# Kernel tuning notes

Hardware: AMD Instinct MI355X
Metric: run time of the kernel (lower is better)

The kernel has to match this reference:

```python
import jax, jax.numpy as jnp
import numpy as np

SPAN_W = 8      # fixed span width (tokens per span)
HID = 150       # Score hidden dim (hardcoded in source)


def _score_mlp(x, w1, b1, w2, b2, w3, b3):
    # Linear->ReLU->(Dropout=id)->Linear->ReLU->(Dropout=id)->Linear ; out dim 1
    h = jax.nn.relu(x @ w1 + b1)
    h = jax.nn.relu(h @ w2 + b2)
    return h @ w3 + b3


def _make_mlp_params(key, in_dim):
    ks = jax.random.split(key, 6)
    s1 = 1.0 / np.sqrt(in_dim)
    s2 = 1.0 / np.sqrt(HID)
    return (
        jax.random.uniform(ks[0], (in_dim, HID), jnp.float32, -s1, s1),
        jax.random.uniform(ks[1], (HID,), jnp.float32, -s1, s1),
        jax.random.uniform(ks[2], (HID, HID), jnp.float32, -s2, s2),
        jax.random.uniform(ks[3], (HID,), jnp.float32, -s2, s2),
        jax.random.uniform(ks[4], (HID, 1), jnp.float32, -s2, s2),
        jax.random.uniform(ks[5], (1,), jnp.float32, -s2, s2),
    )


def setup_inputs() -> dict:
    key = jax.random.key(0)
    k_emb, k_sp, k_a, k_m, k_p = jax.random.split(key, 5)
    E = 768
    B, T, S = 2, 2048, 96
    encoded_docs = jax.random.normal(k_emb, (B, T, E), jnp.float32)
    span_starts = jnp.sort(
        jax.random.randint(k_sp, (B, S), 0, 2040, dtype=jnp.int64), axis=-1)
    aw1, ab1, aw2, ab2, aw3, ab3 = _make_mlp_params(k_a, E)          # attn Score
    mw1, mb1, mw2, mb2, mw3, mb3 = _make_mlp_params(k_m, 3 * E)      # mention Score
    pw1, pb1, pw2, pb2, pw3, pb3 = _make_mlp_params(k_p, 9 * E)      # pair Score
    return {
        "encoded_docs": encoded_docs, "span_starts": span_starts,
        "aw1": aw1, "ab1": ab1, "aw2": aw2, "ab2": ab2, "aw3": aw3, "ab3": ab3,
        "mw1": mw1, "mb1": mb1, "mw2": mw2, "mb2": mb2, "mw3": mw3, "mb3": mb3,
        "pw1": pw1, "pb1": pb1, "pw2": pw2, "pb2": pb2, "pw3": pw3, "pb3": pb3,
    }


def reference(encoded_docs, span_starts,
              aw1, ab1, aw2, ab2, aw3, ab3,
              mw1, mb1, mw2, mb2, mw3, mb3,
              pw1, pb1, pw2, pb2, pw3, pb3):
    B, T, E = encoded_docs.shape
    S = span_starts.shape[1]

    # --- MentionScore ---
    attns = _score_mlp(encoded_docs, aw1, ab1, aw2, ab2, aw3, ab3)  # [B,T,1]
    starts = span_starts                                              # [B,S]
    ends = starts + (SPAN_W - 1)
    g_start = jnp.take_along_axis(encoded_docs, starts[:, :, None], axis=1)  # [B,S,E]
    g_end = jnp.take_along_axis(encoded_docs, ends[:, :, None], axis=1)      # [B,S,E]
    tok_idx = starts[:, :, None] + jnp.arange(SPAN_W, dtype=starts.dtype)     # [B,S,W]
    flat = tok_idx.reshape(B, S * SPAN_W)
    span_emb = jnp.take_along_axis(encoded_docs, flat[:, :, None], axis=1).reshape(B, S, SPAN_W, E)
    span_attn = jnp.take_along_axis(attns, flat[:, :, None], axis=1).reshape(B, S, SPAN_W, 1)
    g_attn = jnp.sum(span_emb * span_attn, axis=2)                    # [B,S,E]
    g_i = jnp.concatenate([g_start, g_end, g_attn], axis=-1)          # [B,S,3E]
    mention_scores = _score_mlp(g_i, mw1, mb1, mw2, mb2, mw3, mb3)    # [B,S,1]

    # --- PairwiseScore: all pairs (i=span_1, j=span_2) ---
    gi = jnp.broadcast_to(g_i[:, :, None, :], (B, S, S, 3 * E))
    gj = jnp.broadcast_to(g_i[:, None, :, :], (B, S, S, 3 * E))
    pair = jnp.concatenate([gi, gj, gi * gj], axis=-1)                # [B,S,S,9E]
    pair_scores = _score_mlp(pair, pw1, pb1, pw2, pb2, pw3, pb3)      # [B,S,S,1]
    ext = (mention_scores[:, :, None, :] + mention_scores[:, None, :, :] + pair_scores) / 3.0
    return jnp.clip(ext, 0.0, 1.0)
```

## Files before the change

### kernel.cpp

```cpp
#include <hip/hip_runtime.h>

#define EDIM   768
#define E3     2304
#define HIDD   150
#define TT     2048
#define SS     96
#define BB     2

typedef unsigned short u16;
using frag   = __attribute__((ext_vector_type(8))) short;
using f32x4v = __attribute__((ext_vector_type(4))) float;
using u16x8  = __attribute__((ext_vector_type(8))) unsigned short;

__device__ __forceinline__ u16 bf16rn(float f) {
    union { float f; unsigned u; } v; v.f = f;
    unsigned r = v.u + 0x7FFF + ((v.u >> 16) & 1);
    return (u16)(r >> 16);
}
__device__ __forceinline__ float bf16tof(u16 h) {
    union { unsigned u; float f; } v; v.u = ((unsigned)h) << 16;
    return v.f;
}
__device__ __forceinline__ void split2(float f, u16& hi, u16& lo) {
    hi = bf16rn(f); lo = bf16rn(f - bf16tof(hi));
}
__device__ __forceinline__ int swzoff(int row, int qd) {
    return row * 32 + (((qd + (row >> 1)) & 3) << 3);
}
__device__ __forceinline__ void async16(const void* g, void* l) {
    __builtin_amdgcn_global_load_lds(
        (const __attribute__((address_space(1))) void*)g,
        (__attribute__((address_space(3))) void*)l, 16, 0, 0);
}

__global__ __launch_bounds__(256) void k_prep_all(
    const float* __restrict__ pw1, const float* __restrict__ mw1,
    const float* __restrict__ aw1, const float* __restrict__ aw2,
    const float* __restrict__ pw2, const float* __restrict__ mw2,
    u16* __restrict__ W12t_hi, u16* __restrict__ W12t_lo,
    u16* __restrict__ AW1t_hi, u16* __restrict__ AW1t_lo,
    u16* __restrict__ AW2t_hi, u16* __restrict__ AW2t_lo,
    u16* __restrict__ PW2t_hi, u16* __restrict__ PW2t_lo,
    u16* __restrict__ MW2t_hi, u16* __restrict__ MW2t_lo)
{
    __shared__ float tile[64][33];
    const int bi = blockIdx.x;
    const int t  = threadIdx.x;

    if (bi < 720) {
        const int k0 = (bi % 36) * 64;
        const int n0 = (bi / 36) * 32;
        const int seg = n0 / 160;
        const int nloc0 = n0 - seg * 160;
        for (int idx = t; idx < 2048; idx += 256) {
            const int kk = idx >> 5, nn = idx & 31;
            const int nl = nloc0 + nn;
            const int k  = k0 + kk;
            float v = 0.f;
            if (nl < HIDD) {
                if (seg == 0)      v = pw1[(long)k * HIDD + nl];
                else if (seg == 1) v = pw1[(long)(E3 + k) * HIDD + nl];
                else if (seg == 2) v = mw1[(long)k * HIDD + nl];
                else               v = pw1[(long)(2 * E3 + k) * HIDD + nl];
            }
            tile[kk][nn] = v;
        }
        __syncthreads();
        for (int idx = t; idx < 2048; idx += 256) {
            const int nn = idx >> 6, kk = idx & 63;
            u16 hi, lo; split2(tile[kk][nn], hi, lo);
            W12t_hi[(long)(n0 + nn) * E3 + k0 + kk] = hi;
            W12t_lo[(long)(n0 + nn) * E3 + k0 + kk] = lo;
        }
    } else if (bi < 1488) {
        const int k = bi - 720;
        if (t < 160) {
            float v = (t < HIDD) ? aw1[k * HIDD + t] : 0.f;
            u16 hi, lo; split2(v, hi, lo);
            AW1t_hi[(long)t * EDIM + k] = hi;
            AW1t_lo[(long)t * EDIM + k] = lo;
        }
    } else {
        const int r = bi - 1488;
        const int k = r % 160;
        const int which = r / 160;
        const float* src = (which == 0) ? aw2 : (which == 1) ? pw2 : mw2;
        u16* dh = (which == 0) ? AW2t_hi : (which == 1) ? PW2t_hi : MW2t_hi;
        u16* dl = (which == 0) ? AW2t_lo : (which == 1) ? PW2t_lo : MW2t_lo;
        if (t < 160) {
            float v = (t < HIDD && k < HIDD) ? src[k * HIDD + t] : 0.f;
            u16 hi, lo; split2(v, hi, lo);
            dh[t * 160 + k] = hi;
            dl[t * 160 + k] = lo;
        }
    }
}

__global__ __launch_bounds__(256) void k_attn1(
    const float* __restrict__ X, const int* __restrict__ spans,
    const u16* __restrict__ AW1t_hi, const u16* __restrict__ AW1t_lo,
    float* __restrict__ AH1)
{
    __shared__ __align__(16) u16 As_hi[32 * 40];
    __shared__ __align__(16) u16 As_lo[32 * 40];
    __shared__ __align__(16) u16 Bs_hi[160 * 40];
    __shared__ __align__(16) u16 Bs_lo[160 * 40];

    const int t    = threadIdx.x;
    const int lane = t & 63;
    const int m    = lane & 15;
    const int quad = lane >> 4;
    const int w    = t >> 6;
    const int mt   = (w & 1) * 16;
    const int nb   = (w >> 1) * 80;
    const int ks   = blockIdx.y;

    const int rr = t >> 3, q = t & 7;
    const int grow = blockIdx.x * 32 + rr;
    const int bs = grow >> 3, sw = grow & 7;
    const int b  = bs / SS;
    const int tok = spans[bs] + sw;
    const float* arow = X + ((long)b * TT + tok) * EDIM;

    f32x4v acc[5];
    #pragma unroll
    for (int ht = 0; ht < 5; ++ht)
        #pragma unroll
        for (int r = 0; r < 4; ++r) acc[ht][r] = 0.f;

    for (int tt = 0; tt < 6; ++tt) {
        const int kk0 = ks * 192 + tt * 32;
        {
            const float4 xv = *(const float4*)&arow[kk0 + q * 4];
            ushort4 hv, lv;
            split2(xv.x, hv.x, lv.x); split2(xv.y, hv.y, lv.y);
            split2(xv.z, hv.z, lv.z); split2(xv.w, hv.w, lv.w);
            *(ushort4*)&As_hi[rr * 40 + q * 4] = hv;
            *(ushort4*)&As_lo[rr * 40 + q * 4] = lv;
        }
        #pragma unroll
        for (int it = 0; it < 3; ++it) {
            const int v = t + it * 256;
            if (v < 640) {
                const int h = v >> 2, qq = v & 3;
                *(uint4*)&Bs_hi[h * 40 + qq * 8] = *(const uint4*)&AW1t_hi[(long)h * EDIM + kk0 + qq * 8];
                *(uint4*)&Bs_lo[h * 40 + qq * 8] = *(const uint4*)&AW1t_lo[(long)h * EDIM + kk0 + qq * 8];
            }
        }
        __syncthreads();
        const frag ah = *(const frag*)&As_hi[(mt + m) * 40 + quad * 8];
        const frag al = *(const frag*)&As_lo[(mt + m) * 40 + quad * 8];
        #pragma unroll
        for (int ht = 0; ht < 5; ++ht) {
            const frag bh = *(const frag*)&Bs_hi[(nb + ht * 16 + m) * 40 + quad * 8];
            const frag bl = *(const frag*)&Bs_lo[(nb + ht * 16 + m) * 40 + quad * 8];
            acc[ht] = __builtin_amdgcn_mfma_f32_16x16x32_bf16(al, bh, acc[ht], 0, 0, 0);
            acc[ht] = __builtin_amdgcn_mfma_f32_16x16x32_bf16(ah, bl, acc[ht], 0, 0, 0);
            acc[ht] = __builtin_amdgcn_mfma_f32_16x16x32_bf16(ah, bh, acc[ht], 0, 0, 0);
        }
        __syncthreads();
    }
    #pragma unroll
    for (int ht = 0; ht < 5; ++ht) {
        #pragma unroll
        for (int r = 0; r < 4; ++r) {
            const int row = blockIdx.x * 32 + mt + quad * 4 + r;
            const int col = nb + ht * 16 + m;
            if (col < HIDD) atomicAdd(&AH1[row * 160 + col], acc[ht][r]);
        }
    }
}

__global__ __launch_bounds__(256) void k_attn2(
    const float* __restrict__ AH1,
    const u16* __restrict__ AW2t_hi, const u16* __restrict__ AW2t_lo,
    const float* __restrict__ ab1, const float* __restrict__ ab2,
    const float* __restrict__ aw3, const float* __restrict__ ab3,
    float* __restrict__ attn_g)
{
    __shared__ __align__(16) u16 As_hi[32 * 40];
    __shared__ __align__(16) u16 As_lo[32 * 40];
    __shared__ __align__(16) u16 Bs_hi[160 * 40];
    __shared__ __align__(16) u16 Bs_lo[160 * 40];
    __shared__ float h1s[32 * 160];
    __shared__ float red[32];

    const int t    = threadIdx.x;
    const int lane = t & 63;
    const int m    = lane & 15;
    const int quad = lane >> 4;
    const int w    = t >> 6;
    const int mt   = (w & 1) * 16;
    const int nb   = (w >> 1) * 80;

    for (int u = t; u < 1280; u += 256) {
        const int row = u / 40, c4 = u - (u / 40) * 40;
        const int c0 = c4 * 4;
        const float4 v = *(const float4*)&AH1[(blockIdx.x * 32 + row) * 160 + c0];
        h1s[row * 160 + c0 + 0] = (c0 + 0 < HIDD) ? fmaxf(v.x + ab1[c0 + 0], 0.f) : 0.f;
        h1s[row * 160 + c0 + 1] = (c0 + 1 < HIDD) ? fmaxf(v.y + ab1[c0 + 1], 0.f) : 0.f;
        h1s[row * 160 + c0 + 2] = (c0 + 2 < HIDD) ? fmaxf(v.z + ab1[c0 + 2], 0.f) : 0.f;
        h1s[row * 160 + c0 + 3] = (c0 + 3 < HIDD) ? fmaxf(v.w + ab1[c0 + 3], 0.f) : 0.f;
    }
    if (t < 32) red[t] = 0.f;
    __syncthreads();

    const int rr = t >> 3, q = t & 7;
    f32x4v acc2[5];
    #pragma unroll
    for (int ht = 0; ht < 5; ++ht)
        #pragma unroll
        for (int r = 0; r < 4; ++r) acc2[ht][r] = 0.f;

    for (int kk = 0; kk < 5; ++kk) {
        {
            const float4 xv = *(const float4*)&h1s[rr * 160 + kk * 32 + q * 4];
            ushort4 hv, lv;
            split2(xv.x, hv.x, lv.x); split2(xv.y, hv.y, lv.y);
            split2(xv.z, hv.z, lv.z); split2(xv.w, hv.w, lv.w);
            *(ushort4*)&As_hi[rr * 40 + q * 4] = hv;
            *(ushort4*)&As_lo[rr * 40 + q * 4] = lv;
        }
        #pragma unroll
        for (int it = 0; it < 3; ++it) {
            const int v = t + it * 256;
            if (v < 640) {
                const int h = v >> 2, qq = v & 3;
                *(uint4*)&Bs_hi[h * 40 + qq * 8] = *(const uint4*)&AW2t_hi[h * 160 + kk * 32 + qq * 8];
                *(uint4*)&Bs_lo[h * 40 + qq * 8] = *(const uint4*)&AW2t_lo[h * 160 + kk * 32 + qq * 8];
            }
        }
        __syncthreads();
        const frag ah = *(const frag*)&As_hi[(mt + m) * 40 + quad * 8];
        const frag al = *(const frag*)&As_lo[(mt + m) * 40 + quad * 8];
        #pragma unroll
        for (int ht = 0; ht < 5; ++ht) {
            const frag bh = *(const frag*)&Bs_hi[(nb + ht * 16 + m) * 40 + quad * 8];
            const frag bl = *(const frag*)&Bs_lo[(nb + ht * 16 + m) * 40 + quad * 8];
            acc2[ht] = __builtin_amdgcn_mfma_f32_16x16x32_bf16(al, bh, acc2[ht], 0, 0, 0);
            acc2[ht] = __builtin_amdgcn_mfma_f32_16x16x32_bf16(ah, bl, acc2[ht], 0, 0, 0);
            acc2[ht] = __builtin_amdgcn_mfma_f32_16x16x32_bf16(ah, bh, acc2[ht], 0, 0, 0);
        }
        __syncthreads();
    }

    float s[4] = {0.f, 0.f, 0.f, 0.f};
    #pragma unroll
    for (int ht = 0; ht < 5; ++ht) {
        const int col = nb + ht * 16 + m;
        if (col < HIDD) {
            const float w3 = aw3[col];
            #pragma unroll
            for (int r = 0; r < 4; ++r)
                s[r] += fmaxf(acc2[ht][r] + ab2[col], 0.f) * w3;
        }
    }
    #pragma unroll
    for (int r = 0; r < 4; ++r) {
        for (int off = 8; off > 0; off >>= 1) s[r] += __shfl_down(s[r], off, 16);
    }
    if (m == 0) {
        #pragma unroll
        for (int r = 0; r < 4; ++r) atomicAdd(&red[mt + quad * 4 + r], s[r]);
    }
    __syncthreads();
    if (t < 32) attn_g[blockIdx.x * 32 + t] = red[t] + ab3[0];
}

__global__ __launch_bounds__(256) void k_span_g(
    const float* __restrict__ X, const int* __restrict__ spans,
    const float* __restrict__ attn_g, float* __restrict__ G_ws,
    u16* __restrict__ Gs_hi, u16* __restrict__ Gs_lo)
{
    __shared__ float a8[8];
    const int t  = threadIdx.x;
    const int bs = blockIdx.x;
    const int b  = bs / SS;
    const int start = spans[bs];
    const float* xb = X + ((long)b * TT + start) * EDIM;
    float* Gp = G_ws + (long)bs * E3;
    u16* Gh = Gs_hi + (long)bs * E3;
    u16* Gl = Gs_lo + (long)bs * E3;
    if (t < 8) a8[t] = attn_g[bs * 8 + t];
    __syncthreads();

    for (int e = t; e < EDIM; e += 256) {
        const float gs = xb[e];
        const float ge = xb[7 * EDIM + e];
        float ga = 0.f;
        #pragma unroll
        for (int w = 0; w < 8; ++w) ga += xb[w * EDIM + e] * a8[w];
        Gp[e] = gs; Gp[EDIM + e] = ge; Gp[2 * EDIM + e] = ga;
        u16 hi, lo;
        split2(gs, hi, lo); Gh[e] = hi;            Gl[e] = lo;
        split2(ge, hi, lo); Gh[EDIM + e] = hi;     Gl[EDIM + e] = lo;
        split2(ga, hi, lo); Gh[2 * EDIM + e] = hi; Gl[2 * EDIM + e] = lo;
    }
}

__global__ __launch_bounds__(256) void k_heavy(
    const float* __restrict__ G_ws,
    const u16* __restrict__ Gs_hi, const u16* __restrict__ Gs_lo,
    const u16* __restrict__ W12t_hi, const u16* __restrict__ W12t_lo,
    const u16* __restrict__ PCt_hi, const u16* __restrict__ PCt_lo,
    float* __restrict__ H1parts, float* __restrict__ UVM)
{
    __shared__ __align__(16) char smem[48128];
    const int id = blockIdx.x;
    const int t  = threadIdx.x;
    const int lane = t & 63;
    const int m    = lane & 15;
    const int quad = lane >> 4;
    const int w    = t >> 6;

    if (id < 576) {
        float* gis  = (float*)smem;
        float* gjst = (float*)(smem + 3072);
        u16* As_hi  = (u16*)(smem + 15360);
        u16* As_lo  = (u16*)(smem + 21504);
        u16* Bs_hi  = (u16*)(smem + 27648);
        u16* Bs_lo  = (u16*)(smem + 37888);

        const int ks = id % 3;
        const int i  = (id / 3) % SS;
        const int b  = id / 288;
        const int ksbase = ks * 768;
        const int jt0 = i >> 4;
        const int ntiles = 6 - jt0;
        const int j0 = jt0 * 16;
        const int R  = 96 - j0;
        const int nI = R >> 3;

        const int hb   = (w & 1) * 80;
        const int apar = w >> 1;
        const int Bl_h = lane >> 2;
        const int Bl_c = lane & 3;
        const int gj_r = lane >> 3;
        const int gj_c = lane & 7;

        const float* Gi = G_ws + (long)(b * SS + i) * E3 + ksbase;
        for (int e = t; e < 768; e += 256) gis[e] = Gi[e];

        f32x4v acc[3][5];
        #pragma unroll
        for (int jt = 0; jt < 3; ++jt)
            #pragma unroll
            for (int ht = 0; ht < 5; ++ht)
                #pragma unroll
                for (int r = 0; r < 4; ++r) acc[jt][ht][r] = 0.f;

        for (int tt = 0; tt < 24; ++tt) {
            const int kk0 = ksbase + tt * 32;
            for (int q2 = w; q2 < 10; q2 += 4) {
                const int h  = q2 * 16 + Bl_h;
                const int qd = (Bl_c - (h >> 1)) & 3;
                const long so = (long)h * E3 + kk0 + qd * 8;
                async16(&PCt_hi[so], &Bs_hi[q2 * 512]);
                async16(&PCt_lo[so], &Bs_lo[q2 * 512]);
            }
            for (int g2 = w; g2 < nI; g2 += 4) {
                const int row = j0 + g2 * 8 + gj_r;
                async16(&G_ws[(long)(b * SS + row) * E3 + kk0 + gj_c * 4],
                        &gjst[g2 * 256]);
            }
            __syncthreads();

            for (int u = t; u < R * 4; u += 256) {
                const int rr = u >> 2, qd = u & 3;
                const float4 g0 = *(const float4*)&gjst[rr * 32 + qd * 8];
                const float4 g1 = *(const float4*)&gjst[rr * 32 + qd * 8 + 4];
                const int kl = tt * 32 + qd * 8;
                u16x8 hv, lv; u16 h, l;
                split2(g0.x * gis[kl + 0], h, l); hv[0] = h; lv[0] = l;
                split2(g0.y * gis[kl + 1], h, l); hv[1] = h; lv[1] = l;
                split2(g0.z * gis[kl + 2], h, l); hv[2] = h; lv[2] = l;
                split2(g0.w * gis[kl + 3], h, l); hv[3] = h; lv[3] = l;
                split2(g1.x * gis[kl + 4], h, l); hv[4] = h; lv[4] = l;
                split2(g1.y * gis[kl + 5], h, l); hv[5] = h; lv[5] = l;
                split2(g1.z * gis[kl + 6], h, l); hv[6] = h; lv[6] = l;
                split2(g1.w * gis[kl + 7], h, l); hv[7] = h; lv[7] = l;
                const int o = swzoff(rr, qd);
                *(u16x8*)&As_hi[o] = hv;
                *(u16x8*)&As_lo[o] = lv;
            }
            __syncthreads();

            frag ah[3], al[3];
            #pragma unroll
            for (int u = 0; u < 3; ++u) {
                const int a = apar + 2 * u;
                if (a < ntiles) {
                    const int o = swzoff(a * 16 + m, quad);
                    ah[u] = *(const frag*)&As_hi[o];
                    al[u] = *(const frag*)&As_lo[o];
                }
            }
            #pragma unroll
            for (int ht = 0; ht < 5; ++ht) {
                const int o = swzoff(hb + ht * 16 + m, quad);
                const frag bh = *(const frag*)&Bs_hi[o];
                const frag bl = *(const frag*)&Bs_lo[o];
                #pragma unroll
                for (int u = 0; u < 3; ++u) {
                    if (apar + 2 * u < ntiles) {
                        acc[u][ht] = __builtin_amdgcn_mfma_f32_16x16x32_bf16(al[u], bh, acc[u][ht], 0, 0, 0);
                        acc[u][ht] = __builtin_amdgcn_mfma_f32_16x16x32_bf16(ah[u], bl, acc[u][ht], 0, 0, 0);
                        acc[u][ht] = __builtin_amdgcn_mfma_f32_16x16x32_bf16(ah[u], bh, acc[u][ht], 0, 0, 0);
                    }
                }
            }
            __syncthreads();
        }

        float* dst = H1parts + (long)ks * ((long)BB * SS * SS * 160);
        #pragma unroll
        for (int u = 0; u < 3; ++u) {
            const int a = apar + 2 * u;
            if (a < ntiles) {
                #pragma unroll
                for (int ht = 0; ht < 5; ++ht) {
                    #pragma unroll
                    for (int r = 0; r < 4; ++r) {
                        const int j = (jt0 + a) * 16 + quad * 4 + r;
                        const int h = hb + ht * 16 + m;
                        dst[((long)(b * SS + i) * SS + j) * 160 + h] = acc[u][ht][r];
                    }
                }
            }
        }
    } else {
        u16* As_hi = (u16*)smem;
        u16* As_lo = (u16*)(smem + 5120);
        u16* Bs_hi = (u16*)(smem + 10240);
        u16* Bs_lo = (u16*)(smem + 23040);

        const int u0 = id - 576;
        const int mb = u0 % 3;
        const int nb = (u0 / 3) % 3;
        const int kz = u0 / 9;
        const int mhalf = (w & 1) * 32;
        const int nbase = (w >> 1) * 80;
        const int arr = t >> 2, aq = t & 3;

        f32x4v acc[2][5];
        #pragma unroll
        for (int i = 0; i < 2; ++i)
            #pragma unroll
            for (int j = 0; j < 5; ++j)
                #pragma unroll
                for (int r = 0; r < 4; ++r) acc[i][j][r] = 0.f;

        for (int tt = 0; tt < 6; ++tt) {
            const int kk0 = kz * 192 + tt * 32;
            *(uint4*)&As_hi[arr * 40 + aq * 8] = *(const uint4*)&Gs_hi[(long)(mb * 64 + arr) * E3 + kk0 + aq * 8];
            *(uint4*)&As_lo[arr * 40 + aq * 8] = *(const uint4*)&Gs_lo[(long)(mb * 64 + arr) * E3 + kk0 + aq * 8];
            #pragma unroll
            for (int it = 0; it < 3; ++it) {
                const int v = t + it * 256;
                if (v < 640) {
                    const int h = v >> 2, qq = v & 3;
                    *(uint4*)&Bs_hi[h * 40 + qq * 8] = *(const uint4*)&W12t_hi[(long)(nb * 160 + h) * E3 + kk0 + qq * 8];
                    *(uint4*)&Bs_lo[h * 40 + qq * 8] = *(const uint4*)&W12t_lo[(long)(nb * 160 + h) * E3 + kk0 + qq * 8];
                }
            }
            __syncthreads();
            frag ah[2], al[2];
            #pragma unroll
            for (int mt = 0; mt < 2; ++mt) {
                ah[mt] = *(const frag*)&As_hi[(mhalf + mt * 16 + m) * 40 + quad * 8];
                al[mt] = *(const frag*)&As_lo[(mhalf + mt * 16 + m) * 40 + quad * 8];
            }
            #pragma unroll
            for (int ht = 0; ht < 5; ++ht) {
                const frag bh = *(const frag*)&Bs_hi[(nbase + ht * 16 + m) * 40 + quad * 8];
                const frag bl = *(const frag*)&Bs_lo[(nbase + ht * 16 + m) * 40 + quad * 8];
                #pragma unroll
                for (int mt = 0; mt < 2; ++mt) {
                    acc[mt][ht] = __builtin_amdgcn_mfma_f32_16x16x32_bf16(al[mt], bh, acc[mt][ht], 0, 0, 0);
                    acc[mt][ht] = __builtin_amdgcn_mfma_f32_16x16x32_bf16(ah[mt], bl, acc[mt][ht], 0, 0, 0);
                    acc[mt][ht] = __builtin_amdgcn_mfma_f32_16x16x32_bf16(ah[mt], bh, acc[mt][ht], 0, 0, 0);
                }
            }
            __syncthreads();
        }
        float* dst = UVM + (long)nb * (192 * 160);
        #pragma unroll
        for (int mt = 0; mt < 2; ++mt) {
            #pragma unroll
            for (int ht = 0; ht < 5; ++ht) {
                #pragma unroll
                for (int r = 0; r < 4; ++r) {
                    const int row = mb * 64 + mhalf + mt * 16 + quad * 4 + r;
                    const int c   = nbase + ht * 16 + m;
                    atomicAdd(&dst[row * 160 + c], acc[mt][ht][r]);
                }
            }
        }
    }
}

__global__ __launch_bounds__(256) void k_pair2(
    const float* __restrict__ H1parts,
    const float* __restrict__ U_ws, const float* __restrict__ V_ws,
    const float* __restrict__ pb1, const float* __restrict__ m_ws,
    const u16* __restrict__ PW2t_hi, const u16* __restrict__ PW2t_lo,
    const float* __restrict__ pb2, const float* __restrict__ pw3,
    const float* __restrict__ pb3,
    float* __restrict__ out)
{
    __shared__ __align__(16) u16 As_hi[32 * 168];
    __shared__ __align__(16) u16 As_lo[32 * 168];
    __shared__ __align__(16) u16 Bs_hi[160 * 40];
    __shared__ __align__(16) u16 Bs_lo[160 * 40];
    __shared__ float uv[160];
    __shared__ float red[32];

    const long partsz = (long)BB * SS * SS * 160;
    const int t  = threadIdx.x;
    const int js = blockIdx.x;
    const int bi = blockIdx.y;
    const int b  = bi / SS;
    const int ii = bi - b * SS;
    const int jb0 = js * 32;

    if (t < 160) uv[t] = U_ws[bi * 160 + t] + ((t < HIDD) ? pb1[t] : 0.f);
    if (t < 32) red[t] = 0.f;
    __syncthreads();

    for (int u = t; u < 32 * 40; u += 256) {
        const int jl = u / 40, hq = u - (u / 40) * 40;
        const int j  = jb0 + jl;
        const int h0 = hq * 4;
        const int mn = ii < j ? ii : j;
        const int mx = ii < j ? j : ii;
        const long idx = (((long)b * SS + mn) * SS + mx) * 160 + h0;
        const float4 vv = *(const float4*)&V_ws[(b * SS + j) * 160 + h0];
        const float4 a0 = *(const float4*)&H1parts[idx];
        const float4 a1 = *(const float4*)&H1parts[partsz + idx];
        const float4 a2 = *(const float4*)&H1parts[2 * partsz + idx];
        const float p0 = fmaxf(a0.x + a1.x + a2.x + vv.x + uv[h0 + 0], 0.f);
        const float p1 = fmaxf(a0.y + a1.y + a2.y + vv.y + uv[h0 + 1], 0.f);
        const float p2 = fmaxf(a0.z + a1.z + a2.z + vv.z + uv[h0 + 2], 0.f);
        const float p3 = fmaxf(a0.w + a1.w + a2.w + vv.w + uv[h0 + 3], 0.f);
        ushort4 hv, lv;
        split2(p0, hv.x, lv.x); split2(p1, hv.y, lv.y);
        split2(p2, hv.z, lv.z); split2(p3, hv.w, lv.w);
        *(ushort4*)&As_hi[jl * 168 + h0] = hv;
        *(ushort4*)&As_lo[jl * 168 + h0] = lv;
    }
    __syncthreads();

    const int lane = t & 63;
    const int m    = lane & 15;
    const int quad = lane >> 4;
    const int w    = t >> 6;
    const int jt   = w >> 1;
    const int nbs  = (w & 1) * 80;

    f32x4v acc[5];
    #pragma unroll
    for (int ht = 0; ht < 5; ++ht)
        #pragma unroll
        for (int r = 0; r < 4; ++r) acc[ht][r] = 0.f;

    for (int kk = 0; kk < 5; ++kk) {
        #pragma unroll
        for (int it = 0; it < 3; ++it) {
            const int v = t + it * 256;
            if (v < 640) {
                const int n = v >> 2, qq = v & 3;
                *(uint4*)&Bs_hi[n * 40 + qq * 8] = *(const uint4*)&PW2t_hi[n * 160 + kk * 32 + qq * 8];
                *(uint4*)&Bs_lo[n * 40 + qq * 8] = *(const uint4*)&PW2t_lo[n * 160 + kk * 32 + qq * 8];
            }
        }
        __syncthreads();
        const frag ah = *(const frag*)&As_hi[(jt * 16 + m) * 168 + kk * 32 + quad * 8];
        const frag al = *(const frag*)&As_lo[(jt * 16 + m) * 168 + kk * 32 + quad * 8];
        #pragma unroll
        for (int ht = 0; ht < 5; ++ht) {
            const frag bh = *(const frag*)&Bs_hi[(nbs + ht * 16 + m) * 40 + quad * 8];
            const frag bl = *(const frag*)&Bs_lo[(nbs + ht * 16 + m) * 40 + quad * 8];
            acc[ht] = __builtin_amdgcn_mfma_f32_16x16x32_bf16(al, bh, acc[ht], 0, 0, 0);
            acc[ht] = __builtin_amdgcn_mfma_f32_16x16x32_bf16(ah, bl, acc[ht], 0, 0, 0);
            acc[ht] = __builtin_amdgcn_mfma_f32_16x16x32_bf16(ah, bh, acc[ht], 0, 0, 0);
        }
        __syncthreads();
    }

    float s[4] = {0.f, 0.f, 0.f, 0.f};
    #pragma unroll
    for (int ht = 0; ht < 5; ++ht) {
        const int col = nbs + ht * 16 + m;
        if (col < HIDD) {
            const float w3 = pw3[col];
            const float b2 = pb2[col];
            #pragma unroll
            for (int r = 0; r < 4; ++r)
                s[r] += fmaxf(acc[ht][r] + b2, 0.f) * w3;
        }
    }
    #pragma unroll
    for (int r = 0; r < 4; ++r)
        for (int off = 8; off > 0; off >>= 1)
            s[r] += __shfl_down(s[r], off, 16);
    if (m == 0) {
        #pragma unroll
        for (int r = 0; r < 4; ++r)
            atomicAdd(&red[jt * 16 + quad * 4 + r], s[r]);
    }
    __syncthreads();

    if (t < 32) {
        const int j = jb0 + t;
        const float sc = red[t] + pb3[0];
        const float v = (m_ws[bi] + m_ws[b * SS + j] + sc) * (1.f / 3.f);
        out[(long)bi * SS + j] = fminf(fmaxf(v, 0.f), 1.f);
    }
}

extern "C" void kernel_launch(void* const* d_in, const int* in_sizes, int n_in,
                              void* d_out, int out_size, void* d_ws, size_t ws_size,
                              hipStream_t stream)
{
    const float* X     = (const float*)d_in[0];
    const int*   spans = (const int*)  d_in[1];
    const float* aw1 = (const float*)d_in[2];
    const float* ab1 = (const float*)d_in[3];
    const float* aw2 = (const float*)d_in[4];
    const float* ab2 = (const float*)d_in[5];
    const float* aw3 = (const float*)d_in[6];
    const float* ab3 = (const float*)d_in[7];
    const float* mw1 = (const float*)d_in[8];
    const float* mb1 = (const float*)d_in[9];
    const float* mw2 = (const float*)d_in[10];
    const float* mb2 = (const float*)d_in[11];
    const float* mw3 = (const float*)d_in[12];
    const float* mb3 = (const float*)d_in[13];
    const float* pw1 = (const float*)d_in[14];
    const float* pb1 = (const float*)d_in[15];
    const float* pw2 = (const float*)d_in[16];
    const float* pb2 = (const float*)d_in[17];
    const float* pw3 = (const float*)d_in[18];
    const float* pb3 = (const float*)d_in[19];
    float* out = (float*)d_out;

    char* p = (char*)d_ws;
    float* attn_g  = (float*)p;  p += 6144;
    float* G_ws    = (float*)p;  p += (long)442368 * 4;
    u16*   Gs_hi   = (u16*)p;    p += (long)442368 * 2;
    u16*   Gs_lo   = (u16*)p;    p += (long)442368 * 2;
    float* UVM     = (float*)p;  p += (long)3 * 192 * 160 * 4;
    float* AH1     = (float*)p;  p += (long)1536 * 160 * 4;
    float* m_ws    = (float*)p;  p += 1024;
    u16*   W12t_hi = (u16*)p;    p += (long)640 * E3 * 2;
    u16*   W12t_lo = (u16*)p;    p += (long)640 * E3 * 2;
    u16*   AW1t_hi = (u16*)p;    p += (long)160 * EDIM * 2;
    u16*   AW1t_lo = (u16*)p;    p += (long)160 * EDIM * 2;
    u16*   AW2t_hi = (u16*)p;    p += 160 * 160 * 2;
    u16*   AW2t_lo = (u16*)p;    p += 160 * 160 * 2;
    u16*   PW2t_hi = (u16*)p;    p += 160 * 160 * 2;
    u16*   PW2t_lo = (u16*)p;    p += 160 * 160 * 2;
    u16*   MW2t_hi = (u16*)p;    p += 160 * 160 * 2;
    u16*   MW2t_lo = (u16*)p;    p += 160 * 160 * 2;
    float* H1parts = (float*)p;

    float* U_ws = UVM;
    float* V_ws = UVM + 192 * 160;
    float* M_ws = UVM + 2 * 192 * 160;
    const u16* PCt_hi = W12t_hi + (long)480 * E3;
    const u16* PCt_lo = W12t_lo + (long)480 * E3;

    hipMemsetAsync(UVM, 0, ((size_t)3 * 192 * 160 + (size_t)1536 * 160) * sizeof(float), stream);

    k_prep_all<<<dim3(1968), 256, 0, stream>>>(pw1, mw1, aw1, aw2, pw2, mw2,
                                               W12t_hi, W12t_lo, AW1t_hi, AW1t_lo,
                                               AW2t_hi, AW2t_lo, PW2t_hi, PW2t_lo,
                                               MW2t_hi, MW2t_lo);

    k_attn1<<<dim3(48, 4), 256, 0, stream>>>(X, spans, AW1t_hi, AW1t_lo, AH1);
    k_attn2<<<dim3(48), 256, 0, stream>>>(AH1, AW2t_hi, AW2t_lo, ab1, ab2, aw3, ab3, attn_g);
    k_span_g<<<dim3(BB * SS), 256, 0, stream>>>(X, spans, attn_g, G_ws, Gs_hi, Gs_lo);

    k_heavy<<<dim3(684), 256, 0, stream>>>(G_ws, Gs_hi, Gs_lo, W12t_hi, W12t_lo,
                                           PCt_hi, PCt_lo, H1parts, UVM);

    k_attn2<<<dim3(6), 256, 0, stream>>>(M_ws, MW2t_hi, MW2t_lo, mb1, mb2, mw3, mb3, m_ws);

    k_pair2<<<dim3(3, BB * SS), 256, 0, stream>>>(
        H1parts, U_ws, V_ws, pb1, m_ws, PW2t_hi, PW2t_lo, pb2, pw3, pb3, out);
}
```

Before: 215.6 us.

## Fuse attention layer-1 GEMM with weight prep into one heterogeneous launch

Splits the aw1 transpose/split into its own small kernel, then merges the attention first-layer GEMM blocks with the remaining weight-prep blocks in one grid. The attention GEMM now uses a 6-way K split (288 blocks) instead of 4-way, so it runs concurrently with independent weight conversion work. This lets the GEMM overlap with prep and gives it more parallelism, at the cost of more atomic adds into AH1 and one extra small launch.

```diff
diff --git a/kernel.cpp b/kernel.cpp
--- a/kernel.cpp
+++ b/kernel.cpp
@@ -33,21 +33,106 @@
         (__attribute__((address_space(3))) void*)l, 16, 0, 0);
 }
 
-__global__ __launch_bounds__(256) void k_prep_all(
+__global__ __launch_bounds__(256) void k_prep_aw1(
+    const float* __restrict__ aw1, u16* __restrict__ W_hi, u16* __restrict__ W_lo)
+{
+    const int k = blockIdx.x, t = threadIdx.x;
+    if (t < 160) {
+        float v = (t < HIDD) ? aw1[k * HIDD + t] : 0.f;
+        u16 hi, lo; split2(v, hi, lo);
+        W_hi[(long)t * EDIM + k] = hi;
+        W_lo[(long)t * EDIM + k] = lo;
+    }
+}
+
+__global__ __launch_bounds__(256) void k_fused1(
+    const float* __restrict__ X, const int* __restrict__ spans,
+    const u16* __restrict__ AW1t_hi, const u16* __restrict__ AW1t_lo,
+    float* __restrict__ AH1,
     const float* __restrict__ pw1, const float* __restrict__ mw1,
-    const float* __restrict__ aw1, const float* __restrict__ aw2,
-    const float* __restrict__ pw2, const float* __restrict__ mw2,
+    const float* __restrict__ aw2, const float* __restrict__ pw2,
+    const float* __restrict__ mw2,
     u16* __restrict__ W12t_hi, u16* __restrict__ W12t_lo,
-    u16* __restrict__ AW1t_hi, u16* __restrict__ AW1t_lo,
     u16* __restrict__ AW2t_hi, u16* __restrict__ AW2t_lo,
     u16* __restrict__ PW2t_hi, u16* __restrict__ PW2t_lo,
     u16* __restrict__ MW2t_hi, u16* __restrict__ MW2t_lo)
 {
-    __shared__ float tile[64][33];
-    const int bi = blockIdx.x;
+    __shared__ __align__(16) char smem[32768];
+    const int id = blockIdx.x;
     const int t  = threadIdx.x;
 
-    if (bi < 720) {
+    if (id < 288) {
+        u16* As_hi = (u16*)smem;
+        u16* As_lo = (u16*)(smem + 2560);
+        u16* Bs_hi = (u16*)(smem + 5120);
+        u16* Bs_lo = (u16*)(smem + 17920);
+
+        const int lane = t & 63;
+        const int m    = lane & 15;
+        const int quad = lane >> 4;
+        const int w    = t >> 6;
+        const int mt   = (w & 1) * 16;
+        const int nb   = (w >> 1) * 80;
+        const int rb   = id % 48;
+        const int ks   = id / 48;
+
+        const int rr = t >> 3, q = t & 7;
+        const int grow = rb * 32 + rr;
+        const int bs = grow >> 3, sw = grow & 7;
+        const int b  = bs / SS;
+        const int tok = spans[bs] + sw;
+        const float* arow = X + ((long)b * TT + tok) * EDIM;
+
+        f32x4v acc[5];
+        #pragma unroll
+        for (int ht = 0; ht < 5; ++ht)
+            #pragma unroll
+            for (int r = 0; r < 4; ++r) acc[ht][r] = 0.f;
+
+        for (int tt = 0; tt < 4; ++tt) {
+            const int kk0 = ks * 128 + tt * 32;
+            {
+                const float4 xv = *(const float4*)&arow[kk0 + q * 4];
+                ushort4 hv, lv;
+                split2(xv.x, hv.x, lv.x); split2(xv.y, hv.y, lv.y);
+                split2(xv.z, hv.z, lv.z); split2(xv.w, hv.w, lv.w);
+                *(ushort4*)&As_hi[rr * 40 + q * 4] = hv;
+                *(ushort4*)&As_lo[rr * 40 + q * 4] = lv;
+            }
+            #pragma unroll
+            for (int it = 0; it < 3; ++it) {
+                const int v = t + it * 256;
+                if (v < 640) {
+                    const int h = v >> 2, qq = v & 3;
+                    *(uint4*)&Bs_hi[h * 40 + qq * 8] = *(const uint4*)&AW1t_hi[(long)h * EDIM + kk0 + qq * 8];
+                    *(uint4*)&Bs_lo[h * 40 + qq * 8] = *(const uint4*)&AW1t_lo[(long)h * EDIM + kk0 + qq * 8];
+                }
+            }
+            __syncthreads();
+            const frag ah = *(const frag*)&As_hi[(mt + m) * 40 + quad * 8];
+            const frag al = *(const frag*)&As_lo[(mt + m) * 40 + quad * 8];
+            #pragma unroll
+            for (int ht = 0; ht < 5; ++ht) {
+                const frag bh = *(const frag*)&Bs_hi[(nb + ht * 16 + m) * 40 + quad * 8];
+                const frag bl = *(const frag*)&Bs_lo[(nb + ht * 16 + m) * 40 + quad * 8];
+                acc[ht] = __builtin_amdgcn_mfma_f32_16x16x32_bf16(al, bh, acc[ht], 0, 0, 0);
+                acc[ht] = __builtin_amdgcn_mfma_f32_16x16x32_bf16(ah, bl, acc[ht], 0, 0, 0);
+                acc[ht] = __builtin_amdgcn_mfma_f32_16x16x32_bf16(ah, bh, acc[ht], 0, 0, 0);
+            }
+            __syncthreads();
+        }
+        #pragma unroll
+        for (int ht = 0; ht < 5; ++ht) {
+            #pragma unroll
+            for (int r = 0; r < 4; ++r) {
+                const int row = rb * 32 + mt + quad * 4 + r;
+                const int col = nb + ht * 16 + m;
+                if (col < HIDD) atomicAdd(&AH1[row * 160 + col], acc[ht][r]);
+            }
+        }
+    } else if (id < 1008) {
+        float (*tile)[33] = (float(*)[33])smem;
+        const int bi = id - 288;
         const int k0 = (bi % 36) * 64;
         const int n0 = (bi / 36) * 32;
         const int seg = n0 / 160;
@@ -72,16 +157,8 @@
             W12t_hi[(long)(n0 + nn) * E3 + k0 + kk] = hi;
             W12t_lo[(long)(n0 + nn) * E3 + k0 + kk] = lo;
         }
-    } else if (bi < 1488) {
-        const int k = bi - 720;
-        if (t < 160) {
-            float v = (t < HIDD) ? aw1[k * HIDD + t] : 0.f;
-            u16 hi, lo; split2(v, hi, lo);
-            AW1t_hi[(long)t * EDIM + k] = hi;
-            AW1t_lo[(long)t * EDIM + k] = lo;
-        }
     } else {
-        const int r = bi - 1488;
+        const int r = id - 1008;
         const int k = r % 160;
         const int which = r / 160;
         const float* src = (which == 0) ? aw2 : (which == 1) ? pw2 : mw2;
@@ -92,81 +169,6 @@
             u16 hi, lo; split2(v, hi, lo);
             dh[t * 160 + k] = hi;
             dl[t * 160 + k] = lo;
-        }
-    }
-}
-
-__global__ __launch_bounds__(256) void k_attn1(
-    const float* __restrict__ X, const int* __restrict__ spans,
-    const u16* __restrict__ AW1t_hi, const u16* __restrict__ AW1t_lo,
-    float* __restrict__ AH1)
-{
-    __shared__ __align__(16) u16 As_hi[32 * 40];
-    __shared__ __align__(16) u16 As_lo[32 * 40];
-    __shared__ __align__(16) u16 Bs_hi[160 * 40];
-    __shared__ __align__(16) u16 Bs_lo[160 * 40];
-
-    const int t    = threadIdx.x;
-    const int lane = t & 63;
-    const int m    = lane & 15;
-    const int quad = lane >> 4;
-    const int w    = t >> 6;
-    const int mt   = (w & 1) * 16;
-    const int nb   = (w >> 1) * 80;
-    const int ks   = blockIdx.y;
-
-    const int rr = t >> 3, q = t & 7;
-    const int grow = blockIdx.x * 32 + rr;
-    const int bs = grow >> 3, sw = grow & 7;
-    const int b  = bs / SS;
-    const int tok = spans[bs] + sw;
-    const float* arow = X + ((long)b * TT + tok) * EDIM;
-
-    f32x4v acc[5];
-    #pragma unroll
-    for (int ht = 0; ht < 5; ++ht)
-        #pragma unroll
-        for (int r = 0; r < 4; ++r) acc[ht][r] = 0.f;
-
-    for (int tt = 0; tt < 6; ++tt) {
-        const int kk0 = ks * 192 + tt * 32;
-        {
-            const float4 xv = *(const float4*)&arow[kk0 + q * 4];
-            ushort4 hv, lv;
-            split2(xv.x, hv.x, lv.x); split2(xv.y, hv.y, lv.y);
-            split2(xv.z, hv.z, lv.z); split2(xv.w, hv.w, lv.w);
-            *(ushort4*)&As_hi[rr * 40 + q * 4] = hv;
-            *(ushort4*)&As_lo[rr * 40 + q * 4] = lv;
-        }
-        #pragma unroll
-        for (int it = 0; it < 3; ++it) {
-            const int v = t + it * 256;
-            if (v < 640) {
-                const int h = v >> 2, qq = v & 3;
-                *(uint4*)&Bs_hi[h * 40 + qq * 8] = *(const uint4*)&AW1t_hi[(long)h * EDIM + kk0 + qq * 8];
-                *(uint4*)&Bs_lo[h * 40 + qq * 8] = *(const uint4*)&AW1t_lo[(long)h * EDIM + kk0 + qq * 8];
-            }
-        }
-        __syncthreads();
-        const frag ah = *(const frag*)&As_hi[(mt + m) * 40 + quad * 8];
-        const frag al = *(const frag*)&As_lo[(mt + m) * 40 + quad * 8];
-        #pragma unroll
-        for (int ht = 0; ht < 5; ++ht) {
-            const frag bh = *(const frag*)&Bs_hi[(nb + ht * 16 + m) * 40 + quad * 8];
-            const frag bl = *(const frag*)&Bs_lo[(nb + ht * 16 + m) * 40 + quad * 8];
-            acc[ht] = __builtin_amdgcn_mfma_f32_16x16x32_bf16(al, bh, acc[ht], 0, 0, 0);
-            acc[ht] = __builtin_amdgcn_mfma_f32_16x16x32_bf16(ah, bl, acc[ht], 0, 0, 0);
-            acc[ht] = __builtin_amdgcn_mfma_f32_16x16x32_bf16(ah, bh, acc[ht], 0, 0, 0);
-        }
-        __syncthreads();
-    }
-    #pragma unroll
-    for (int ht = 0; ht < 5; ++ht) {
-        #pragma unroll
-        for (int r = 0; r < 4; ++r) {
-            const int row = blockIdx.x * 32 + mt + quad * 4 + r;
-            const int col = nb + ht * 16 + m;
-            if (col < HIDD) atomicAdd(&AH1[row * 160 + col], acc[ht][r]);
         }
     }
 }
@@ -672,12 +674,13 @@
 
     hipMemsetAsync(UVM, 0, ((size_t)3 * 192 * 160 + (size_t)1536 * 160) * sizeof(float), stream);
 
-    k_prep_all<<<dim3(1968), 256, 0, stream>>>(pw1, mw1, aw1, aw2, pw2, mw2,
-                                               W12t_hi, W12t_lo, AW1t_hi, AW1t_lo,
-                                               AW2t_hi, AW2t_lo, PW2t_hi, PW2t_lo,
-                                               MW2t_hi, MW2t_lo);
-
-    k_attn1<<<dim3(48, 4), 256, 0, stream>>>(X, spans, AW1t_hi, AW1t_lo, AH1);
+    k_prep_aw1<<<dim3(EDIM), 256, 0, stream>>>(aw1, AW1t_hi, AW1t_lo);
+
+    k_fused1<<<dim3(1488), 256, 0, stream>>>(X, spans, AW1t_hi, AW1t_lo, AH1,
+                                             pw1, mw1, aw2, pw2, mw2,
+                                             W12t_hi, W12t_lo, AW2t_hi, AW2t_lo,
+                                             PW2t_hi, PW2t_lo, MW2t_hi, MW2t_lo);
+
     k_attn2<<<dim3(48), 256, 0, stream>>>(AH1, AW2t_hi, AW2t_lo, ab1, ab2, aw3, ab3, attn_g);
     k_span_g<<<dim3(BB * SS), 256, 0, stream>>>(X, spans, attn_g, G_ws, Gs_hi, Gs_lo);
 
```

Result: no change. 213.9 us (-0.8%).
